# Performance work log

Measured on AMD Instinct MI355X. Metric: run time of the kernel, lower is better.

## Reference

```python
import jax, jax.numpy as jnp
import numpy as np

N = 128   # system size (number of sequential RNN steps)
B = 8192  # batch of samples
H = 128   # hidden units per layer (units=[128,128])
D = 2     # input_dim (spin up/down one-hot)


def setup_inputs() -> dict:
    key = jax.random.key(0)
    ks = jax.random.split(key, 11)
    s = 1.0 / np.sqrt(H)  # torch nn.RNNCell/Linear default U(-1/sqrt(H), 1/sqrt(H))
    bits = jax.random.randint(ks[0], (N, B), 0, D)
    samples = jax.nn.one_hot(bits, D, dtype=jnp.float32)  # (N, B, D) one-hot spins
    u = lambda k, shp: jax.random.uniform(k, shp, jnp.float32, -s, s)
    return {
        "samples": samples,
        "W_ih0": u(ks[1], (H, D)), "b_ih0": u(ks[2], (H,)),
        "W_hh0": u(ks[3], (H, H)), "b_hh0": u(ks[4], (H,)),
        "W_ih1": u(ks[5], (H, H)), "b_ih1": u(ks[6], (H,)),
        "W_hh1": u(ks[7], (H, H)), "b_hh1": u(ks[8], (H,)),
        "W_dense": u(ks[9], (D, H)), "b_dense": u(ks[10], (D,)),
    }


def reference(samples, W_ih0, b_ih0, W_hh0, b_hh0,
              W_ih1, b_ih1, W_hh1, b_hh1, W_dense, b_dense):
    # Faithful jax port of RNN_wavefunction.log_prob:
    # p_t = <softmax(dense(h1_t)), s_t>; returns sum_t log p_t with shape (1, B).
    # For one-hot s_t, log(sum(prob*s_t)) == sum(s_t * log_softmax(logits)) (stable form).
    Bsz = samples.shape[1]
    # input at step t is the sampled spin from step t-1; zeros at t=0
    inputs = jnp.concatenate(
        [jnp.zeros((1, Bsz, D), samples.dtype), samples[:-1]], axis=0)
    h0 = jnp.zeros((Bsz, H), samples.dtype)
    h1 = jnp.zeros((Bsz, H), samples.dtype)

    def step(carry, xs):
        h0, h1 = carry
        x_t, s_t = xs  # x_t: (B, D) prev spin one-hot, s_t: (B, D) current spin
        # nn.RNNCell: h' = tanh(x W_ih^T + b_ih + h W_hh^T + b_hh)
        h0 = jnp.tanh(x_t @ W_ih0.T + b_ih0 + h0 @ W_hh0.T + b_hh0)
        h1 = jnp.tanh(h0 @ W_ih1.T + b_ih1 + h1 @ W_hh1.T + b_hh1)
        logits = h1 @ W_dense.T + b_dense           # (B, 2)
        logp = jax.nn.log_softmax(logits, axis=-1)
        lp_t = jnp.sum(logp * s_t, axis=-1)          # (B,) = log p(s_t)
        return (h0, h1), lp_t

    _, lps = jax.lax.scan(step, (h0, h1), (inputs, samples))  # lps: (N, B)
    return jnp.sum(lps, axis=0, keepdims=True)  # (1, B), matches torch keepdim=True
```

## Files before the change

### kernel.cpp

```cpp
#include <hip/hip_runtime.h>
#include <hip/hip_bf16.h>


#define NSTEP 128
#define BTOT  8192
#define HID   128
#define SPB   32
#define NBLK  (BTOT / SPB)
#define NTHR  512

typedef __attribute__((ext_vector_type(8))) short bf16x8;
typedef __attribute__((ext_vector_type(4))) float f32x4;
typedef __attribute__((ext_vector_type(2))) float f32x2;
typedef __attribute__((ext_vector_type(2))) unsigned uint32x2;

__device__ __forceinline__ short f2bf(float v) {
    unsigned u = __builtin_bit_cast(unsigned, v);
    u += 0x7FFFu + ((u >> 16) & 1u);
    return (short)(u >> 16);
}
__device__ __forceinline__ unsigned cvt2bf(float a, float b) {
    __hip_bfloat162 h2 = __float22bfloat162_rn(make_float2(a, b));
    unsigned u; __builtin_memcpy(&u, &h2, sizeof(u));
    return u;
}
__device__ __forceinline__ f32x2 tanh2(f32x2 x) {
    f32x2 z = x * 2.885390081777927f;
    float e0 = __builtin_exp2f(z.x);
    float e1 = __builtin_exp2f(z.y);
    f32x2 d = {e0 + 1.0f, e1 + 1.0f};
    float r = __builtin_amdgcn_rcpf(d.x * d.y);
    f32x2 inv = {r * d.y, r * d.x};
    return inv * -2.0f + 1.0f;
}

__global__ __launch_bounds__(NTHR, 2) void rnn_wf_kernel(
    const float* __restrict__ samples,
    const float* __restrict__ Wih0,
    const float* __restrict__ bih0,
    const float* __restrict__ Whh0,
    const float* __restrict__ bhh0,
    const float* __restrict__ Wih1,
    const float* __restrict__ bih1,
    const float* __restrict__ Whh1,
    const float* __restrict__ bhh1,
    const float* __restrict__ Wd,
    const float* __restrict__ bd,
    float* __restrict__ out)
{
    __shared__ short sH0A[2][16 * HID];
    __shared__ short sH1A[2][16 * HID];
    __shared__ short sH0B[2][16 * HID];
    __shared__ short sH1B[2][16 * HID];
    __shared__ unsigned sMask[NSTEP];
    __shared__ float sLd[2][NSTEP * 17];
    __shared__ __attribute__((aligned(16))) float sBias[4 * HID];
    __shared__ __attribute__((aligned(16))) short sFwd[4 * 64 * 8];

    const int tid  = threadIdx.x;
    const int b0   = blockIdx.x * SPB;
    const int w    = tid >> 6;
    const int lane = tid & 63;
    const int q    = lane >> 4;
    const int c    = lane & 15;

    if (tid < NSTEP) {
        unsigned msk = 0;
        #pragma unroll
        for (int m = 0; m < SPB; ++m) {
            float e1 = samples[((size_t)tid * BTOT + b0 + m) * 2 + 1];
            if (e1 > 0.5f) msk |= (1u << m);
        }
        sMask[tid] = msk;
    }
    if (tid >= NSTEP && tid < NSTEP + HID) {
        const int n = tid - NSTEP;
        const float bb = bih0[n] + bhh0[n];
        sBias[n]       = bb + Wih0[n * 2 + 0];
        sBias[128 + n] = bb + Wih0[n * 2 + 1];
        sBias[256 + n] = bih1[n] + bhh1[n];
        sBias[384 + n] = bb;
    }
    if (tid >= 256 && tid < 512) {
        const int t2 = tid - 256;
        const int kb = t2 >> 6, l = t2 & 63, cc = l & 15, qq = l >> 4;
        bf16x8 v;
        #pragma unroll
        for (int j = 0; j < 8; ++j)
            v[j] = (cc < 2) ? f2bf(Wd[cc * HID + kb * 32 + qq * 8 + j]) : (short)0;
        *reinterpret_cast<bf16x8*>(&sFwd[(kb * 64 + l) * 8]) = v;
    }

    bf16x8 fhh0[4], fih1[4], fhh1[4];
    {
        const int nn = w * 16 + c;
        #pragma unroll
        for (int kb = 0; kb < 4; ++kb) {
            const int off = nn * HID + kb * 32 + q * 8;
            bf16x8 v0, v1, v2;
            #pragma unroll
            for (int j = 0; j < 8; ++j) {
                v0[j] = f2bf(Whh0[off + j]);
                v1[j] = f2bf(Wih1[off + j]);
                v2[j] = f2bf(Whh1[off + j]);
            }
            fhh0[kb] = v0; fih1[kb] = v1; fhh1[kb] = v2;
        }
    }
    const float bd0 = bd[0], bd1 = bd[1];

    int ra[4];
    #pragma unroll
    for (int kb = 0; kb < 4; ++kb)
        ra[kb] = c * HID + (((kb * 4 + q) ^ c) << 3);
    const int wa = c * HID + (((2 * w + (q >> 1)) ^ c) << 3) + ((q & 1) << 2);
    const int ib = w * 16 + q * 4;

    bool bmPrevA = false, bmPrevB = false;

    auto storeL = [&](short* buf, const f32x4& a) {
        f32x2 t0 = tanh2((f32x2){a[0], a[1]});
        f32x2 t1 = tanh2((f32x2){a[2], a[3]});
        uint32x2 v = {cvt2bf(t0.x, t0.y), cvt2bf(t1.x, t1.y)};
        *reinterpret_cast<uint32x2*>(&buf[wa]) = v;
    };

    __syncthreads();

    {
        f32x4 bv = *reinterpret_cast<const f32x4*>(&sBias[384 + ib]);
        storeL(sH0A[1], bv);
        storeL(sH0B[1], bv);
    }
    __syncthreads();

    {
        const unsigned msk = sMask[0];
        const bool bmA = (msk >> c) & 1u;
        const bool bmB = (msk >> (16 + c)) & 1u;
        const float* bpA = bmA ? (sBias + 128) : sBias;
        const float* bpB = bmB ? (sBias + 128) : sBias;
        f32x4 a0A = *reinterpret_cast<const f32x4*>(&bpA[ib]);
        f32x4 a0B = *reinterpret_cast<const f32x4*>(&bpB[ib]);
        f32x4 a1A = *reinterpret_cast<const f32x4*>(&sBias[256 + ib]);
        f32x4 a1B = a1A;
        #pragma unroll
        for (int kb = 0; kb < 4; ++kb) {
            bf16x8 f0A = *reinterpret_cast<const bf16x8*>(&sH0A[1][ra[kb]]);
            bf16x8 f0B = *reinterpret_cast<const bf16x8*>(&sH0B[1][ra[kb]]);
            a0A = __builtin_amdgcn_mfma_f32_16x16x32_bf16(fhh0[kb], f0A, a0A, 0, 0, 0);
            a0B = __builtin_amdgcn_mfma_f32_16x16x32_bf16(fhh0[kb], f0B, a0B, 0, 0, 0);
            a1A = __builtin_amdgcn_mfma_f32_16x16x32_bf16(fih1[kb], f0A, a1A, 0, 0, 0);
            a1B = __builtin_amdgcn_mfma_f32_16x16x32_bf16(fih1[kb], f0B, a1B, 0, 0, 0);
        }
        storeL(sH0A[0], a0A);
        storeL(sH1A[0], a1A);
        storeL(sH0B[0], a0B);
        storeL(sH1B[0], a1B);
        bmPrevA = bmA; bmPrevB = bmB;
        __syncthreads();
    }

    auto stepMain = [&](int i,
                        const short* r0A, const short* r1A, short* w0A, short* w1A,
                        const short* r0B, const short* r1B, short* w0B, short* w1B) {
        const unsigned msk = sMask[i - 1];
        const bool bmA = (msk >> c) & 1u;
        const bool bmB = (msk >> (16 + c)) & 1u;
        const float* bpA = bmA ? (sBias + 128) : sBias;
        const float* bpB = bmB ? (sBias + 128) : sBias;
        f32x4 a0A = *reinterpret_cast<const f32x4*>(&bpA[ib]);
        f32x4 a0B = *reinterpret_cast<const f32x4*>(&bpB[ib]);
        f32x4 a1A = *reinterpret_cast<const f32x4*>(&sBias[256 + ib]);
        f32x4 a1B = a1A;
        bf16x8 f0A[4], f1A[4], f0B[4], f1B[4];
        #pragma unroll
        for (int kb = 0; kb < 4; ++kb) {
            f0A[kb] = *reinterpret_cast<const bf16x8*>(&r0A[ra[kb]]);
            f1A[kb] = *reinterpret_cast<const bf16x8*>(&r1A[ra[kb]]);
            f0B[kb] = *reinterpret_cast<const bf16x8*>(&r0B[ra[kb]]);
            f1B[kb] = *reinterpret_cast<const bf16x8*>(&r1B[ra[kb]]);
        }
        #pragma unroll
        for (int kb = 0; kb < 4; ++kb) {
            a0A = __builtin_amdgcn_mfma_f32_16x16x32_bf16(fhh0[kb], f0A[kb], a0A, 0, 0, 0);
            a0B = __builtin_amdgcn_mfma_f32_16x16x32_bf16(fhh0[kb], f0B[kb], a0B, 0, 0, 0);
            a1A = __builtin_amdgcn_mfma_f32_16x16x32_bf16(fhh1[kb], f1A[kb], a1A, 0, 0, 0);
            a1B = __builtin_amdgcn_mfma_f32_16x16x32_bf16(fhh1[kb], f1B[kb], a1B, 0, 0, 0);
        }
        #pragma unroll
        for (int kb = 0; kb < 4; ++kb) {
            a1A = __builtin_amdgcn_mfma_f32_16x16x32_bf16(fih1[kb], f0A[kb], a1A, 0, 0, 0);
            a1B = __builtin_amdgcn_mfma_f32_16x16x32_bf16(fih1[kb], f0B[kb], a1B, 0, 0, 0);
        }
        if (w == (i & 7)) {
            f32x4 aL = {bd0, bd1, 0.f, 0.f};
            #pragma unroll
            for (int kb = 0; kb < 4; ++kb) {
                bf16x8 fw = *reinterpret_cast<const bf16x8*>(&sFwd[(kb * 64 + lane) * 8]);
                aL = __builtin_amdgcn_mfma_f32_16x16x32_bf16(fw, f1A[kb], aL, 0, 0, 0);
            }
            if (q == 0)
                sLd[0][(i - 2) * 17 + c] = bmPrevA ? (aL[0] - aL[1]) : (aL[1] - aL[0]);
        }
        if (w == ((i + 4) & 7)) {
            f32x4 aL = {bd0, bd1, 0.f, 0.f};
            #pragma unroll
            for (int kb = 0; kb < 4; ++kb) {
                bf16x8 fw = *reinterpret_cast<const bf16x8*>(&sFwd[(kb * 64 + lane) * 8]);
                aL = __builtin_amdgcn_mfma_f32_16x16x32_bf16(fw, f1B[kb], aL, 0, 0, 0);
            }
            if (q == 0)
                sLd[1][(i - 2) * 17 + c] = bmPrevB ? (aL[0] - aL[1]) : (aL[1] - aL[0]);
        }
        bmPrevA = bmA; bmPrevB = bmB;
        storeL(w0A, a0A);
        storeL(w1A, a1A);
        storeL(w0B, a0B);
        storeL(w1B, a1B);
        __syncthreads();
    };

    for (int i = 2; i < NSTEP; i += 2) {
        stepMain(i,
                 sH0A[0], sH1A[0], sH0A[1], sH1A[1],
                 sH0B[0], sH1B[0], sH0B[1], sH1B[1]);
        stepMain(i + 1,
                 sH0A[1], sH1A[1], sH0A[0], sH1A[0],
                 sH0B[1], sH1B[1], sH0B[0], sH1B[0]);
    }

    {
        f32x4 a1A = *reinterpret_cast<const f32x4*>(&sBias[256 + ib]);
        f32x4 a1B = a1A;
        bf16x8 f0A[4], f1A[4], f0B[4], f1B[4];
        #pragma unroll
        for (int kb = 0; kb < 4; ++kb) {
            f0A[kb] = *reinterpret_cast<const bf16x8*>(&sH0A[0][ra[kb]]);
            f1A[kb] = *reinterpret_cast<const bf16x8*>(&sH1A[0][ra[kb]]);
            f0B[kb] = *reinterpret_cast<const bf16x8*>(&sH0B[0][ra[kb]]);
            f1B[kb] = *reinterpret_cast<const bf16x8*>(&sH1B[0][ra[kb]]);
        }
        #pragma unroll
        for (int kb = 0; kb < 4; ++kb) {
            a1A = __builtin_amdgcn_mfma_f32_16x16x32_bf16(fhh1[kb], f1A[kb], a1A, 0, 0, 0);
            a1B = __builtin_amdgcn_mfma_f32_16x16x32_bf16(fhh1[kb], f1B[kb], a1B, 0, 0, 0);
        }
        #pragma unroll
        for (int kb = 0; kb < 4; ++kb) {
            a1A = __builtin_amdgcn_mfma_f32_16x16x32_bf16(fih1[kb], f0A[kb], a1A, 0, 0, 0);
            a1B = __builtin_amdgcn_mfma_f32_16x16x32_bf16(fih1[kb], f0B[kb], a1B, 0, 0, 0);
        }
        if (w == 0) {
            f32x4 aL = {bd0, bd1, 0.f, 0.f};
            #pragma unroll
            for (int kb = 0; kb < 4; ++kb) {
                bf16x8 fw = *reinterpret_cast<const bf16x8*>(&sFwd[(kb * 64 + lane) * 8]);
                aL = __builtin_amdgcn_mfma_f32_16x16x32_bf16(fw, f1A[kb], aL, 0, 0, 0);
            }
            if (q == 0)
                sLd[0][126 * 17 + c] = bmPrevA ? (aL[0] - aL[1]) : (aL[1] - aL[0]);
        }
        if (w == 4) {
            f32x4 aL = {bd0, bd1, 0.f, 0.f};
            #pragma unroll
            for (int kb = 0; kb < 4; ++kb) {
                bf16x8 fw = *reinterpret_cast<const bf16x8*>(&sFwd[(kb * 64 + lane) * 8]);
                aL = __builtin_amdgcn_mfma_f32_16x16x32_bf16(fw, f1B[kb], aL, 0, 0, 0);
            }
            if (q == 0)
                sLd[1][126 * 17 + c] = bmPrevB ? (aL[0] - aL[1]) : (aL[1] - aL[0]);
        }
        storeL(sH1A[1], a1A);
        storeL(sH1B[1], a1B);
        __syncthreads();
    }
    if (w == 1) {
        f32x4 aL = {bd0, bd1, 0.f, 0.f};
        #pragma unroll
        for (int kb = 0; kb < 4; ++kb) {
            bf16x8 f1 = *reinterpret_cast<const bf16x8*>(&sH1A[1][ra[kb]]);
            bf16x8 fw = *reinterpret_cast<const bf16x8*>(&sFwd[(kb * 64 + lane) * 8]);
            aL = __builtin_amdgcn_mfma_f32_16x16x32_bf16(fw, f1, aL, 0, 0, 0);
        }
        if (q == 0) {
            const bool bit = (sMask[NSTEP - 1] >> c) & 1u;
            sLd[0][127 * 17 + c] = bit ? (aL[0] - aL[1]) : (aL[1] - aL[0]);
        }
    }
    if (w == 5) {
        f32x4 aL = {bd0, bd1, 0.f, 0.f};
        #pragma unroll
        for (int kb = 0; kb < 4; ++kb) {
            bf16x8 f1 = *reinterpret_cast<const bf16x8*>(&sH1B[1][ra[kb]]);
            bf16x8 fw = *reinterpret_cast<const bf16x8*>(&sFwd[(kb * 64 + lane) * 8]);
            aL = __builtin_amdgcn_mfma_f32_16x16x32_bf16(fw, f1, aL, 0, 0, 0);
        }
        if (q == 0) {
            const bool bit = (sMask[NSTEP - 1] >> (16 + c)) & 1u;
            sLd[1][127 * 17 + c] = bit ? (aL[0] - aL[1]) : (aL[1] - aL[0]);
        }
    }
    __syncthreads();

    {
        const int s  = tid >> 4;
        const int k  = tid & 15;
        const int tb = s >> 4;
        const int si = s & 15;
        float acc = 0.0f;
        #pragma unroll
        for (int j = 0; j < 8; ++j) {
            const float x = sLd[tb][(j * 16 + k) * 17 + si];
            const float ed = __builtin_exp2f(x * 1.4426950408889634f);
            acc -= 0.6931471805599453f * __builtin_log2f(1.0f + ed);
        }
        #pragma unroll
        for (int off = 1; off < 16; off <<= 1)
            acc += __shfl_xor(acc, off, 64);
        if (k == 0)
            out[b0 + s] = acc;
    }
}

extern "C" void kernel_launch(void* const* d_in, const int* in_sizes, int n_in,
                              void* d_out, int out_size, void* d_ws, size_t ws_size,
                              hipStream_t stream) {
    rnn_wf_kernel<<<NBLK, NTHR, 0, stream>>>(
        (const float*)d_in[0],
        (const float*)d_in[1],
        (const float*)d_in[2],
        (const float*)d_in[3],
        (const float*)d_in[4],
        (const float*)d_in[5],
        (const float*)d_in[6],
        (const float*)d_in[7],
        (const float*)d_in[8],
        (const float*)d_in[9],
        (const float*)d_in[10],
        (float*)d_out);
}
```

Baseline: 251.5 us.

## Serialize A/B half-tile processing to cut registers and raise occupancy to 4 blocks

```diff
diff --git a/kernel.cpp b/kernel.cpp
--- a/kernel.cpp
+++ b/kernel.cpp
@@ -34,7 +34,7 @@
     return inv * -2.0f + 1.0f;
 }
 
-__global__ __launch_bounds__(NTHR, 2) void rnn_wf_kernel(
+__global__ __launch_bounds__(NTHR, 4) void rnn_wf_kernel(
     const float* __restrict__ samples,
     const float* __restrict__ Wih0,
     const float* __restrict__ bih0,
@@ -136,28 +136,36 @@
 
     {
         const unsigned msk = sMask[0];
-        const bool bmA = (msk >> c) & 1u;
-        const bool bmB = (msk >> (16 + c)) & 1u;
-        const float* bpA = bmA ? (sBias + 128) : sBias;
-        const float* bpB = bmB ? (sBias + 128) : sBias;
-        f32x4 a0A = *reinterpret_cast<const f32x4*>(&bpA[ib]);
-        f32x4 a0B = *reinterpret_cast<const f32x4*>(&bpB[ib]);
-        f32x4 a1A = *reinterpret_cast<const f32x4*>(&sBias[256 + ib]);
-        f32x4 a1B = a1A;
-        #pragma unroll
-        for (int kb = 0; kb < 4; ++kb) {
-            bf16x8 f0A = *reinterpret_cast<const bf16x8*>(&sH0A[1][ra[kb]]);
-            bf16x8 f0B = *reinterpret_cast<const bf16x8*>(&sH0B[1][ra[kb]]);
-            a0A = __builtin_amdgcn_mfma_f32_16x16x32_bf16(fhh0[kb], f0A, a0A, 0, 0, 0);
-            a0B = __builtin_amdgcn_mfma_f32_16x16x32_bf16(fhh0[kb], f0B, a0B, 0, 0, 0);
-            a1A = __builtin_amdgcn_mfma_f32_16x16x32_bf16(fih1[kb], f0A, a1A, 0, 0, 0);
-            a1B = __builtin_amdgcn_mfma_f32_16x16x32_bf16(fih1[kb], f0B, a1B, 0, 0, 0);
-        }
-        storeL(sH0A[0], a0A);
-        storeL(sH1A[0], a1A);
-        storeL(sH0B[0], a0B);
-        storeL(sH1B[0], a1B);
-        bmPrevA = bmA; bmPrevB = bmB;
+        {
+            const bool bmA = (msk >> c) & 1u;
+            const float* bpA = bmA ? (sBias + 128) : sBias;
+            f32x4 a0A = *reinterpret_cast<const f32x4*>(&bpA[ib]);
+            f32x4 a1A = *reinterpret_cast<const f32x4*>(&sBias[256 + ib]);
+            #pragma unroll
+            for (int kb = 0; kb < 4; ++kb) {
+                bf16x8 f0A = *reinterpret_cast<const bf16x8*>(&sH0A[1][ra[kb]]);
+                a0A = __builtin_amdgcn_mfma_f32_16x16x32_bf16(fhh0[kb], f0A, a0A, 0, 0, 0);
+                a1A = __builtin_amdgcn_mfma_f32_16x16x32_bf16(fih1[kb], f0A, a1A, 0, 0, 0);
+            }
+            storeL(sH0A[0], a0A);
+            storeL(sH1A[0], a1A);
+            bmPrevA = bmA;
+        }
+        {
+            const bool bmB = (msk >> (16 + c)) & 1u;
+            const float* bpB = bmB ? (sBias + 128) : sBias;
+            f32x4 a0B = *reinterpret_cast<const f32x4*>(&bpB[ib]);
+            f32x4 a1B = *reinterpret_cast<const f32x4*>(&sBias[256 + ib]);
+            #pragma unroll
+            for (int kb = 0; kb < 4; ++kb) {
+                bf16x8 f0B = *reinterpret_cast<const bf16x8*>(&sH0B[1][ra[kb]]);
+                a0B = __builtin_amdgcn_mfma_f32_16x16x32_bf16(fhh0[kb], f0B, a0B, 0, 0, 0);
+                a1B = __builtin_amdgcn_mfma_f32_16x16x32_bf16(fih1[kb], f0B, a1B, 0, 0, 0);
+            }
+            storeL(sH0B[0], a0B);
+            storeL(sH1B[0], a1B);
+            bmPrevB = bmB;
+        }
         __syncthreads();
     }
 
@@ -165,59 +173,72 @@
                         const short* r0A, const short* r1A, short* w0A, short* w1A,
                         const short* r0B, const short* r1B, short* w0B, short* w1B) {
         const unsigned msk = sMask[i - 1];
-        const bool bmA = (msk >> c) & 1u;
-        const bool bmB = (msk >> (16 + c)) & 1u;
-        const float* bpA = bmA ? (sBias + 128) : sBias;
-        const float* bpB = bmB ? (sBias + 128) : sBias;
-        f32x4 a0A = *reinterpret_cast<const f32x4*>(&bpA[ib]);
-        f32x4 a0B = *reinterpret_cast<const f32x4*>(&bpB[ib]);
-        f32x4 a1A = *reinterpret_cast<const f32x4*>(&sBias[256 + ib]);
-        f32x4 a1B = a1A;
-        bf16x8 f0A[4], f1A[4], f0B[4], f1B[4];
-        #pragma unroll
-        for (int kb = 0; kb < 4; ++kb) {
-            f0A[kb] = *reinterpret_cast<const bf16x8*>(&r0A[ra[kb]]);
-            f1A[kb] = *reinterpret_cast<const bf16x8*>(&r1A[ra[kb]]);
-            f0B[kb] = *reinterpret_cast<const bf16x8*>(&r0B[ra[kb]]);
-            f1B[kb] = *reinterpret_cast<const bf16x8*>(&r1B[ra[kb]]);
-        }
-        #pragma unroll
-        for (int kb = 0; kb < 4; ++kb) {
-            a0A = __builtin_amdgcn_mfma_f32_16x16x32_bf16(fhh0[kb], f0A[kb], a0A, 0, 0, 0);
-            a0B = __builtin_amdgcn_mfma_f32_16x16x32_bf16(fhh0[kb], f0B[kb], a0B, 0, 0, 0);
-            a1A = __builtin_amdgcn_mfma_f32_16x16x32_bf16(fhh1[kb], f1A[kb], a1A, 0, 0, 0);
-            a1B = __builtin_amdgcn_mfma_f32_16x16x32_bf16(fhh1[kb], f1B[kb], a1B, 0, 0, 0);
-        }
-        #pragma unroll
-        for (int kb = 0; kb < 4; ++kb) {
-            a1A = __builtin_amdgcn_mfma_f32_16x16x32_bf16(fih1[kb], f0A[kb], a1A, 0, 0, 0);
-            a1B = __builtin_amdgcn_mfma_f32_16x16x32_bf16(fih1[kb], f0B[kb], a1B, 0, 0, 0);
-        }
-        if (w == (i & 7)) {
-            f32x4 aL = {bd0, bd1, 0.f, 0.f};
-            #pragma unroll
-            for (int kb = 0; kb < 4; ++kb) {
-                bf16x8 fw = *reinterpret_cast<const bf16x8*>(&sFwd[(kb * 64 + lane) * 8]);
-                aL = __builtin_amdgcn_mfma_f32_16x16x32_bf16(fw, f1A[kb], aL, 0, 0, 0);
-            }
-            if (q == 0)
-                sLd[0][(i - 2) * 17 + c] = bmPrevA ? (aL[0] - aL[1]) : (aL[1] - aL[0]);
-        }
-        if (w == ((i + 4) & 7)) {
-            f32x4 aL = {bd0, bd1, 0.f, 0.f};
-            #pragma unroll
-            for (int kb = 0; kb < 4; ++kb) {
-                bf16x8 fw = *reinterpret_cast<const bf16x8*>(&sFwd[(kb * 64 + lane) * 8]);
-                aL = __builtin_amdgcn_mfma_f32_16x16x32_bf16(fw, f1B[kb], aL, 0, 0, 0);
-            }
-            if (q == 0)
-                sLd[1][(i - 2) * 17 + c] = bmPrevB ? (aL[0] - aL[1]) : (aL[1] - aL[0]);
-        }
-        bmPrevA = bmA; bmPrevB = bmB;
-        storeL(w0A, a0A);
-        storeL(w1A, a1A);
-        storeL(w0B, a0B);
-        storeL(w1B, a1B);
+        {
+            const bool bmA = (msk >> c) & 1u;
+            const float* bpA = bmA ? (sBias + 128) : sBias;
+            f32x4 a0A = *reinterpret_cast<const f32x4*>(&bpA[ib]);
+            f32x4 a1A = *reinterpret_cast<const f32x4*>(&sBias[256 + ib]);
+            bf16x8 f0A[4], f1A[4];
+            #pragma unroll
+            for (int kb = 0; kb < 4; ++kb) {
+                f0A[kb] = *reinterpret_cast<const bf16x8*>(&r0A[ra[kb]]);
+                f1A[kb] = *reinterpret_cast<const bf16x8*>(&r1A[ra[kb]]);
+            }
+            #pragma unroll
+            for (int kb = 0; kb < 4; ++kb) {
+                a0A = __builtin_amdgcn_mfma_f32_16x16x32_bf16(fhh0[kb], f0A[kb], a0A, 0, 0, 0);
+                a1A = __builtin_amdgcn_mfma_f32_16x16x32_bf16(fhh1[kb], f1A[kb], a1A, 0, 0, 0);
+            }
+            #pragma unroll
+            for (int kb = 0; kb < 4; ++kb)
+                a1A = __builtin_amdgcn_mfma_f32_16x16x32_bf16(fih1[kb], f0A[kb], a1A, 0, 0, 0);
+            if (w == (i & 7)) {
+                f32x4 aL = {bd0, bd1, 0.f, 0.f};
+                #pragma unroll
+                for (int kb = 0; kb < 4; ++kb) {
+                    bf16x8 fw = *reinterpret_cast<const bf16x8*>(&sFwd[(kb * 64 + lane) * 8]);
+                    aL = __builtin_amdgcn_mfma_f32_16x16x32_bf16(fw, f1A[kb], aL, 0, 0, 0);
+                }
+                if (q == 0)
+                    sLd[0][(i - 2) * 17 + c] = bmPrevA ? (aL[0] - aL[1]) : (aL[1] - aL[0]);
+            }
+            bmPrevA = bmA;
+            storeL(w0A, a0A);
+            storeL(w1A, a1A);
+        }
+        {
+            const bool bmB = (msk >> (16 + c)) & 1u;
+            const float* bpB = bmB ? (sBias + 128) : sBias;
+            f32x4 a0B = *reinterpret_cast<const f32x4*>(&bpB[ib]);
+            f32x4 a1B = *reinterpret_cast<const f32x4*>(&sBias[256 + ib]);
+            bf16x8 f0B[4], f1B[4];
+            #pragma unroll
+            for (int kb = 0; kb < 4; ++kb) {
+                f0B[kb] = *reinterpret_cast<const bf16x8*>(&r0B[ra[kb]]);
+                f1B[kb] = *reinterpret_cast<const bf16x8*>(&r1B[ra[kb]]);
+            }
+            #pragma unroll
+            for (int kb = 0; kb < 4; ++kb) {
+                a0B = __builtin_amdgcn_mfma_f32_16x16x32_bf16(fhh0[kb], f0B[kb], a0B, 0, 0, 0);
+                a1B = __builtin_amdgcn_mfma_f32_16x16x32_bf16(fhh1[kb], f1B[kb], a1B, 0, 0, 0);
+            }
+            #pragma unroll
+            for (int kb = 0; kb < 4; ++kb)
+                a1B = __builtin_amdgcn_mfma_f32_16x16x32_bf16(fih1[kb], f0B[kb], a1B, 0, 0, 0);
+            if (w == ((i + 4) & 7)) {
+                f32x4 aL = {bd0, bd1, 0.f, 0.f};
+                #pragma unroll
+                for (int kb = 0; kb < 4; ++kb) {
+                    bf16x8 fw = *reinterpret_cast<const bf16x8*>(&sFwd[(kb * 64 + lane) * 8]);
+                    aL = __builtin_amdgcn_mfma_f32_16x16x32_bf16(fw, f1B[kb], aL, 0, 0, 0);
+                }
+                if (q == 0)
+                    sLd[1][(i - 2) * 17 + c] = bmPrevB ? (aL[0] - aL[1]) : (aL[1] - aL[0]);
+            }
+            bmPrevB = bmB;
+            storeL(w0B, a0B);
+            storeL(w1B, a1B);
+        }
         __syncthreads();
     };
 
@@ -231,48 +252,58 @@
     }
 
     {
-        f32x4 a1A = *reinterpret_cast<const f32x4*>(&sBias[256 + ib]);
-        f32x4 a1B = a1A;
-        bf16x8 f0A[4], f1A[4], f0B[4], f1B[4];
-        #pragma unroll
-        for (int kb = 0; kb < 4; ++kb) {
-            f0A[kb] = *reinterpret_cast<const bf16x8*>(&sH0A[0][ra[kb]]);
-            f1A[kb] = *reinterpret_cast<const bf16x8*>(&sH1A[0][ra[kb]]);
-            f0B[kb] = *reinterpret_cast<const bf16x8*>(&sH0B[0][ra[kb]]);
-            f1B[kb] = *reinterpret_cast<const bf16x8*>(&sH1B[0][ra[kb]]);
-        }
-        #pragma unroll
-        for (int kb = 0; kb < 4; ++kb) {
-            a1A = __builtin_amdgcn_mfma_f32_16x16x32_bf16(fhh1[kb], f1A[kb], a1A, 0, 0, 0);
-            a1B = __builtin_amdgcn_mfma_f32_16x16x32_bf16(fhh1[kb], f1B[kb], a1B, 0, 0, 0);
-        }
-        #pragma unroll
-        for (int kb = 0; kb < 4; ++kb) {
-            a1A = __builtin_amdgcn_mfma_f32_16x16x32_bf16(fih1[kb], f0A[kb], a1A, 0, 0, 0);
-            a1B = __builtin_amdgcn_mfma_f32_16x16x32_bf16(fih1[kb], f0B[kb], a1B, 0, 0, 0);
-        }
-        if (w == 0) {
-            f32x4 aL = {bd0, bd1, 0.f, 0.f};
-            #pragma unroll
-            for (int kb = 0; kb < 4; ++kb) {
-                bf16x8 fw = *reinterpret_cast<const bf16x8*>(&sFwd[(kb * 64 + lane) * 8]);
-                aL = __builtin_amdgcn_mfma_f32_16x16x32_bf16(fw, f1A[kb], aL, 0, 0, 0);
-            }
-            if (q == 0)
-                sLd[0][126 * 17 + c] = bmPrevA ? (aL[0] - aL[1]) : (aL[1] - aL[0]);
-        }
-        if (w == 4) {
-            f32x4 aL = {bd0, bd1, 0.f, 0.f};
-            #pragma unroll
-            for (int kb = 0; kb < 4; ++kb) {
-                bf16x8 fw = *reinterpret_cast<const bf16x8*>(&sFwd[(kb * 64 + lane) * 8]);
-                aL = __builtin_amdgcn_mfma_f32_16x16x32_bf16(fw, f1B[kb], aL, 0, 0, 0);
-            }
-            if (q == 0)
-                sLd[1][126 * 17 + c] = bmPrevB ? (aL[0] - aL[1]) : (aL[1] - aL[0]);
-        }
-        storeL(sH1A[1], a1A);
-        storeL(sH1B[1], a1B);
+        {
+            f32x4 a1A = *reinterpret_cast<const f32x4*>(&sBias[256 + ib]);
+            bf16x8 f0A[4], f1A[4];
+            #pragma unroll
+            for (int kb = 0; kb < 4; ++kb) {
+                f0A[kb] = *reinterpret_cast<const bf16x8*>(&sH0A[0][ra[kb]]);
+                f1A[kb] = *reinterpret_cast<const bf16x8*>(&sH1A[0][ra[kb]]);
+            }
+            #pragma unroll
+            for (int kb = 0; kb < 4; ++kb)
+                a1A = __builtin_amdgcn_mfma_f32_16x16x32_bf16(fhh1[kb], f1A[kb], a1A, 0, 0, 0);
+            #pragma unroll
+            for (int kb = 0; kb < 4; ++kb)
+                a1A = __builtin_amdgcn_mfma_f32_16x16x32_bf16(fih1[kb], f0A[kb], a1A, 0, 0, 0);
+            if (w == 0) {
+                f32x4 aL = {bd0, bd1, 0.f, 0.f};
+                #pragma unroll
+                for (int kb = 0; kb < 4; ++kb) {
+                    bf16x8 fw = *reinterpret_cast<const bf16x8*>(&sFwd[(kb * 64 + lane) * 8]);
+                    aL = __builtin_amdgcn_mfma_f32_16x16x32_bf16(fw, f1A[kb], aL, 0, 0, 0);
+                }
+                if (q == 0)
+                    sLd[0][126 * 17 + c] = bmPrevA ? (aL[0] - aL[1]) : (aL[1] - aL[0]);
+            }
+            storeL(sH1A[1], a1A);
+        }
+        {
+            f32x4 a1B = *reinterpret_cast<const f32x4*>(&sBias[256 + ib]);
+            bf16x8 f0B[4], f1B[4];
+            #pragma unroll
+            for (int kb = 0; kb < 4; ++kb) {
+                f0B[kb] = *reinterpret_cast<const bf16x8*>(&sH0B[0][ra[kb]]);
+                f1B[kb] = *reinterpret_cast<const bf16x8*>(&sH1B[0][ra[kb]]);
+            }
+            #pragma unroll
+            for (int kb = 0; kb < 4; ++kb)
+                a1B = __builtin_amdgcn_mfma_f32_16x16x32_bf16(fhh1[kb], f1B[kb], a1B, 0, 0, 0);
+            #pragma unroll
+            for (int kb = 0; kb < 4; ++kb)
+                a1B = __builtin_amdgcn_mfma_f32_16x16x32_bf16(fih1[kb], f0B[kb], a1B, 0, 0, 0);
+            if (w == 4) {
+                f32x4 aL = {bd0, bd1, 0.f, 0.f};
+                #pragma unroll
+                for (int kb = 0; kb < 4; ++kb) {
+                    bf16x8 fw = *reinterpret_cast<const bf16x8*>(&sFwd[(kb * 64 + lane) * 8]);
+                    aL = __builtin_amdgcn_mfma_f32_16x16x32_bf16(fw, f1B[kb], aL, 0, 0, 0);
+                }
+                if (q == 0)
+                    sLd[1][126 * 17 + c] = bmPrevB ? (aL[0] - aL[1]) : (aL[1] - aL[0]);
+            }
+            storeL(sH1B[1], a1B);
+        }
         __syncthreads();
     }
     if (w == 1) {
```

Result: slower. 257.8 us (+2.5%).
